# Performance work log

Measured on AMD Instinct MI355X. Metric: run time of the kernel, lower is better.

The kernel has to match this reference:

```python
import jax, jax.numpy as jnp
import numpy as np

N_ENT = 40000      # n_ent_vocab
NUM_POS = 24       # n_rel_vocab // 2
N_REL = 48         # n_rel_vocab (fwd + inverse relations)
BODY_LEN = 3
N_EDGES = 300000
BATCH = 64
THR = 1e-20


def setup_inputs() -> dict:
    key = jax.random.key(0)
    ks = jax.random.split(key, 8)
    return {
        "q_head": jax.random.randint(ks[0], (BATCH,), 0, N_ENT, dtype=jnp.int32),
        "q_rel": jax.random.randint(ks[1], (BATCH,), 0, NUM_POS, dtype=jnp.int32),
        "t": jax.random.randint(ks[2], (BATCH,), 0, N_ENT, dtype=jnp.int32),
        # dec_output is a softmax over relations -> positive weights in (0,1)
        "attention": jax.random.uniform(ks[3], (BATCH, BODY_LEN, N_REL), dtype=jnp.float32),
        "edge_head": jax.random.randint(ks[4], (N_EDGES,), 0, N_ENT, dtype=jnp.int32),
        "edge_tail": jax.random.randint(ks[5], (N_EDGES,), 0, N_ENT, dtype=jnp.int32),
        "edge_rel": jax.random.randint(ks[6], (N_EDGES,), 0, NUM_POS, dtype=jnp.int32),
        # uncertain-KG confidence values stored in the sparse adjacency
        "edge_val": jax.random.uniform(ks[7], (N_EDGES,), dtype=jnp.float32),
    }


def reference(q_head, q_rel, t, attention, edge_head, edge_tail, edge_rel, edge_val):
    """Fused equivalent of Translator.forwardAllNLP.

    database[r] are sparse [N_ENT, N_ENT] matrices; here the whole multigraph is
    one edge list (edge_head, edge_tail, edge_rel, edge_val). torch.sparse.mm
    per relation + attention-weighted accumulation becomes a single gather /
    segment_sum pass over all relations at once.
    """
    B = q_head.shape[0]
    # zero out the query triples in the (shared) database, as in the torch code
    killed = ((edge_head[None, :] == q_head[:, None])
              & (edge_tail[None, :] == t[:, None])
              & (edge_rel[None, :] == q_rel[:, None])).any(axis=0)
    vals = jnp.where(killed, 0.0, edge_val)  # [E]

    mem = jax.nn.one_hot(q_head, N_ENT, dtype=jnp.float32)  # [B, N_ENT]
    for step in range(BODY_LEN):
        attn = attention[:, step]                 # [B, N_REL]
        a_fwd = attn[:, edge_rel]                 # [B, E]  attention[:,step,r]
        a_rev = attn[:, edge_rel + NUM_POS]       # [B, E]  attention[:,step,r+num_pos]
        gh = mem[:, edge_head] * vals             # [B, E]  sparse.mm(mem, A_r)
        gt = mem[:, edge_tail] * vals             # [B, E]  sparse.mm(mem, A_r^T)
        fwd_msg = jax.ops.segment_sum((gh * a_fwd).T, edge_tail, num_segments=N_ENT).T
        rev_msg = jax.ops.segment_sum((gt * a_rev).T, edge_head, num_segments=N_ENT).T
        # self-loop term: memories * attention[:, step, -1]
        mem = fwd_msg + rev_msg + mem * attn[:, -1:]

    mem = mem / jnp.maximum(THR, mem.sum(axis=1, keepdims=True))
    # -sum(one_hot(t) * log(max(thr, mem))) == -log(max(thr, mem[b, t[b]]))
    tgt_prob = mem[jnp.arange(B), t]
    batch_loss = -jnp.log(jnp.maximum(THR, tgt_prob)).mean()
    return batch_loss, mem
```

## Files before the change

### kernel.cpp

```cpp
#include <hip/hip_runtime.h>
#include <hip/hip_bf16.h>

#define N_ENT 40000
#define NB 64
#define BODY_LEN 3
#define N_REL 48
#define NUM_POS 24
#define THR 1e-20f

#define SCAN_NBLK ((N_ENT + 255) / 256)


__global__ void k_zero(int* __restrict__ deg, int* __restrict__ fcnt,
                       float* __restrict__ sums) {
    int i = blockIdx.x * 256 + threadIdx.x;
    if (i < N_ENT) deg[i] = 0;
    if (i < 3) fcnt[i] = 0;
    if (i >= 64 && i < 128) sums[i - 64] = 0.0f;
}

__global__ void k_count(const int* __restrict__ eh, const int* __restrict__ et,
                        int* __restrict__ deg, int nE) {
    int i = blockIdx.x * 256 + threadIdx.x;
    if (i < nE) {
        atomicAdd(&deg[eh[i]], 1);
        atomicAdd(&deg[et[i]], 1);
    }
}

__global__ void k_blocksum(const int* __restrict__ deg, int* __restrict__ partial) {
    __shared__ int ws[4];
    int t = threadIdx.x;
    int i = blockIdx.x * 256 + t;
    int v = (i < N_ENT) ? deg[i] : 0;
#pragma unroll
    for (int off = 32; off > 0; off >>= 1) v += __shfl_down(v, off);
    if ((t & 63) == 0) ws[t >> 6] = v;
    __syncthreads();
    if (t == 0) partial[blockIdx.x] = ws[0] + ws[1] + ws[2] + ws[3];
}

__global__ void k_scan_small(const int* __restrict__ partial, int* __restrict__ pofs,
                             int* __restrict__ offs) {
    __shared__ int s[256];
    int t = threadIdx.x;
    int v = (t < SCAN_NBLK) ? partial[t] : 0;
    s[t] = v;
    __syncthreads();
    for (int off = 1; off < 256; off <<= 1) {
        int add = (t >= off) ? s[t - off] : 0;
        __syncthreads();
        s[t] += add;
        __syncthreads();
    }
    if (t < SCAN_NBLK) pofs[t] = s[t] - v;
    if (t == 255) offs[N_ENT] = s[255];
}

__global__ void k_offsets(const int* __restrict__ deg, const int* __restrict__ pofs,
                          int* __restrict__ offs, int* __restrict__ csrCur) {
    __shared__ int s[256];
    int t = threadIdx.x;
    int i = blockIdx.x * 256 + t;
    int v = (i < N_ENT) ? deg[i] : 0;
    s[t] = v;
    __syncthreads();
    for (int off = 1; off < 256; off <<= 1) {
        int add = (t >= off) ? s[t - off] : 0;
        __syncthreads();
        s[t] += add;
        __syncthreads();
    }
    if (i < N_ENT) {
        int ex = pofs[blockIdx.x] + s[t] - v;
        offs[i] = ex;
        csrCur[i] = ex;
    }
}

__global__ void k_scatter(const int* __restrict__ qh, const int* __restrict__ qr,
                          const int* __restrict__ tt, const int* __restrict__ eh,
                          const int* __restrict__ et, const int* __restrict__ er,
                          const float* __restrict__ ev, int* __restrict__ csrCur,
                          uint2* __restrict__ csr, int nE) {
    __shared__ long long s_key[NB];
    int tid = threadIdx.x;
    if (tid < NB)
        s_key[tid] = ((long long)qh[tid] << 32) | ((long long)tt[tid] << 8) | (long long)qr[tid];
    __syncthreads();
    int i = blockIdx.x * 256 + tid;
    if (i < nE) {
        int h = eh[i], t = et[i], r = er[i];
        long long k = ((long long)h << 32) | ((long long)t << 8) | (long long)r;
        bool killed = false;
#pragma unroll
        for (int b = 0; b < NB; ++b) killed |= (s_key[b] == k);
        float v = killed ? 0.0f : ev[i];
        unsigned vb = __float_as_uint(v);
        int sh = atomicAdd(&csrCur[h], 1);
        csr[sh] = make_uint2((unsigned)t | ((unsigned)r << 16), vb);
        int st = atomicAdd(&csrCur[t], 1);
        csr[st] = make_uint2((unsigned)h | ((unsigned)(r + NUM_POS) << 16), vb);
    }
}

#define DEC_BLOCKS 320
#define FLIST_LDS 192

__device__ __forceinline__ void flag_entities(unsigned long long m, int lane,
                                              int ent, int* s_cnt, int* s_list) {
    bool flag = ((lane & 15) == 0) && ((m >> lane) & 0xFFFFULL);
    unsigned long long am = __ballot(flag);
    if (am) {
        int leader = __ffsll((long long)am) - 1;
        int lb = 0;
        if (lane == leader) lb = atomicAdd(s_cnt, __popcll(am));
        lb = __shfl(lb, leader);
        if (flag) {
            int rank = __popcll(am & ((1ULL << lane) - 1ULL));
            s_list[lb + rank] = ent;
        }
    }
}

__global__ void k_init_decay(const int* __restrict__ qh, const float* __restrict__ attn,
                             float* __restrict__ nxt, int* __restrict__ fcnt,
                             int* __restrict__ flist) {
    __shared__ float s_d[NB];
    __shared__ int s_q[NB];
    __shared__ int s_list[FLIST_LDS];
    __shared__ int s_cnt, s_gbase;
    int tid = threadIdx.x;
    if (tid < NB) {
        s_d[tid] = attn[tid * (BODY_LEN * N_REL) + 0 * N_REL + (N_REL - 1)];
        s_q[tid] = qh[tid];
    }
    if (tid == 0) s_cnt = 0;
    __syncthreads();
    int lane = tid & 63;
    const int total4 = NB * N_ENT / 4;
    for (int i4 = blockIdx.x * 256 + tid; i4 < total4; i4 += gridDim.x * 256) {
        int ent = (i4 * 4) >> 6;
        int b0 = (i4 * 4) & 63;
        float4 w;
        w.x = (s_q[b0 + 0] == ent) ? s_d[b0 + 0] : 0.0f;
        w.y = (s_q[b0 + 1] == ent) ? s_d[b0 + 1] : 0.0f;
        w.z = (s_q[b0 + 2] == ent) ? s_d[b0 + 2] : 0.0f;
        w.w = (s_q[b0 + 3] == ent) ? s_d[b0 + 3] : 0.0f;
        ((float4*)nxt)[i4] = w;
        bool nz = (s_q[b0 + 0] == ent) | (s_q[b0 + 1] == ent) |
                  (s_q[b0 + 2] == ent) | (s_q[b0 + 3] == ent);
        unsigned long long m = __ballot(nz);
        flag_entities(m, lane, ent, &s_cnt, s_list);
    }
    __syncthreads();
    if (tid == 0 && s_cnt) s_gbase = atomicAdd(fcnt, s_cnt);
    __syncthreads();
    for (int i = tid; i < s_cnt; i += 256) flist[s_gbase + i] = s_list[i];
}

__global__ void k_decay(const float* __restrict__ oldm, float* __restrict__ nxt,
                        const float* __restrict__ attn, int step,
                        int* __restrict__ fcnt, int* __restrict__ flist) {
    __shared__ float s_d[NB];
    __shared__ int s_list[FLIST_LDS];
    __shared__ int s_cnt, s_gbase;
    int tid = threadIdx.x;
    if (tid < NB)
        s_d[tid] = attn[tid * (BODY_LEN * N_REL) + step * N_REL + (N_REL - 1)];
    if (tid == 0) s_cnt = 0;
    __syncthreads();
    int lane = tid & 63;
    const int total4 = NB * N_ENT / 4;
    for (int i4 = blockIdx.x * 256 + tid; i4 < total4; i4 += gridDim.x * 256) {
        float4 v = ((const float4*)oldm)[i4];
        int b0 = (tid * 4) & 63;
        float4 w;
        w.x = v.x * s_d[b0 + 0];
        w.y = v.y * s_d[b0 + 1];
        w.z = v.z * s_d[b0 + 2];
        w.w = v.w * s_d[b0 + 3];
        ((float4*)nxt)[i4] = w;
        bool nz = (v.x != 0.0f) | (v.y != 0.0f) | (v.z != 0.0f) | (v.w != 0.0f);
        unsigned long long m = __ballot(nz);
        flag_entities(m, lane, (i4 * 4) >> 6, &s_cnt, s_list);
    }
    __syncthreads();
    if (tid == 0 && s_cnt) s_gbase = atomicAdd(fcnt, s_cnt);
    __syncthreads();
    for (int i = tid; i < s_cnt; i += 256) flist[s_gbase + i] = s_list[i];
}

template <bool STEP0>
__global__ __launch_bounds__(256) void k_fstep(
    const uint2* __restrict__ csr, const int* __restrict__ offs,
    const int* __restrict__ flist, const int* __restrict__ fcnt,
    const float* __restrict__ attn, int step,
    const float* __restrict__ oldm, const int* __restrict__ qh,
    float* __restrict__ nxt) {
    __shared__ float s_attn[NB][N_REL + 1];
    int tid = threadIdx.x;
    for (int idx = tid; idx < NB * N_REL; idx += 256) {
        int b = idx / N_REL, r = idx % N_REL;
        s_attn[b][r] = attn[b * (BODY_LEN * N_REL) + step * N_REL + r];
    }
    __syncthreads();
    int lane = tid & 63;
    int myqh = STEP0 ? qh[lane] : 0;
    int n = *fcnt;
    int w = (blockIdx.x * 256 + tid) >> 6;
    int nW = (gridDim.x * 256) >> 6;
    for (int f = w; f < n; f += nW) {
        int e = flist[f];
        float src = STEP0 ? ((myqh == e) ? 1.0f : 0.0f)
                          : oldm[(size_t)e * 64 + lane];
        int base = offs[e];
        int cnt = offs[e + 1] - base;
        for (int k0 = 0; k0 < cnt; k0 += 64) {
            uint2 slot = make_uint2(0u, 0u);
            if (k0 + lane < cnt) slot = csr[base + k0 + lane];
            int lim = min(64, cnt - k0);
            for (int j = 0; j < lim; ++j) {
                unsigned meta = (unsigned)__shfl((int)slot.x, j);
                float v = __uint_as_float((unsigned)__shfl((int)slot.y, j));
                if (v == 0.0f) continue;
                float val = src * v * s_attn[lane][meta >> 16];
                if (val != 0.0f)
                    atomicAdd(&nxt[(size_t)(meta & 0xFFFFu) * 64 + lane], val);
            }
        }
    }
}

__global__ void k_sums(const float* __restrict__ mem, float* __restrict__ sums) {
    __shared__ float s_s[NB];
    if (threadIdx.x < NB) s_s[threadIdx.x] = 0.0f;
    __syncthreads();
    const float4* m4 = (const float4*)mem;
    const int total4 = NB * N_ENT / 4;
    float4 acc = {0.0f, 0.0f, 0.0f, 0.0f};
    for (int i = blockIdx.x * 256 + threadIdx.x; i < total4; i += gridDim.x * 256) {
        float4 v = m4[i];
        acc.x += v.x; acc.y += v.y; acc.z += v.z; acc.w += v.w;
    }
    int b0 = (threadIdx.x * 4) & 63;
    atomicAdd(&s_s[b0 + 0], acc.x);
    atomicAdd(&s_s[b0 + 1], acc.y);
    atomicAdd(&s_s[b0 + 2], acc.z);
    atomicAdd(&s_s[b0 + 3], acc.w);
    __syncthreads();
    if (threadIdx.x < NB) atomicAdd(&sums[threadIdx.x], s_s[threadIdx.x]);
}

__global__ void k_norm_tr(const float* __restrict__ mem, const float* __restrict__ sums,
                          const int* __restrict__ tt, float* __restrict__ out) {
    if (blockIdx.x == N_ENT / 64) {
        int b = threadIdx.x;
        if (b < 64) {
            float p = mem[(size_t)tt[b] * 64 + b] / fmaxf(THR, sums[b]);
            float l = -logf(fmaxf(THR, p));
#pragma unroll
            for (int off = 32; off > 0; off >>= 1) l += __shfl_down(l, off);
            if (b == 0) out[0] = l * (1.0f / 64.0f);
        }
        return;
    }
    __shared__ float tile[64][65];
    __shared__ float s_inv[64];
    int tid = threadIdx.x;
    int e0 = blockIdx.x * 64;
    if (tid < 64) s_inv[tid] = 1.0f / fmaxf(THR, sums[tid]);
    const float4* m4 = (const float4*)(mem + (size_t)e0 * 64);
#pragma unroll
    for (int k = 0; k < 4; ++k) {
        int i4 = k * 256 + tid;
        float4 v = m4[i4];
        int el = i4 >> 4, b0 = (i4 * 4) & 63;
        tile[el][b0 + 0] = v.x; tile[el][b0 + 1] = v.y;
        tile[el][b0 + 2] = v.z; tile[el][b0 + 3] = v.w;
    }
    __syncthreads();
#pragma unroll
    for (int k = 0; k < 16; ++k) {
        int idx = k * 256 + tid;
        int el = idx & 63, b = idx >> 6;
        out[1 + (size_t)b * N_ENT + e0 + el] = tile[el][b] * s_inv[b];
    }
}

extern "C" void kernel_launch(void* const* d_in, const int* in_sizes, int n_in,
                              void* d_out, int out_size, void* d_ws, size_t ws_size,
                              hipStream_t stream) {
    const int*   qh   = (const int*)d_in[0];
    const int*   qr   = (const int*)d_in[1];
    const int*   tt   = (const int*)d_in[2];
    const float* attn = (const float*)d_in[3];
    const int*   eh   = (const int*)d_in[4];
    const int*   et   = (const int*)d_in[5];
    const int*   er   = (const int*)d_in[6];
    const float* ev   = (const float*)d_in[7];
    float* out = (float*)d_out;
    int nE = in_sizes[4];

    const size_t MEM_BYTES = (size_t)NB * N_ENT * sizeof(float);
    char* ws = (char*)d_ws;
    int*   offs    = (int*)ws;
    int*   deg     = (int*)(ws + (192u << 10));
    int*   csrCur  = (int*)(ws + (384u << 10));
    int*   flist   = (int*)(ws + (576u << 10));
    int*   fcnt    = (int*)(ws + (768u << 10));
    float* sums    = (float*)(ws + (768u << 10) + 256);
    int*   partial = (int*)(ws + (768u << 10) + 4096);
    int*   pofs    = (int*)(ws + (768u << 10) + 8192);
    float* memA    = (float*)(ws + (1u << 20));
    float* memB;
    char*  csrBase;
    size_t csrBytes = (size_t)2 * nE * sizeof(uint2);
    size_t needBoth = (size_t)(1u << 20) + 2 * MEM_BYTES + csrBytes;
    if (ws_size >= needBoth) {
        memB = (float*)(ws + (1u << 20) + MEM_BYTES);
        csrBase = ws + (1u << 20) + 2 * MEM_BYTES;
    } else {
        memB = out + 1;
        csrBase = ws + (1u << 20) + MEM_BYTES;
    }
    uint2* csr = (uint2*)csrBase;

    const int EB = (nE + 255) / 256;

    k_zero<<<SCAN_NBLK, 256, 0, stream>>>(deg, fcnt, sums);
    k_count<<<EB, 256, 0, stream>>>(eh, et, deg, nE);
    k_blocksum<<<SCAN_NBLK, 256, 0, stream>>>(deg, partial);
    k_scan_small<<<1, 256, 0, stream>>>(partial, pofs, offs);
    k_offsets<<<SCAN_NBLK, 256, 0, stream>>>(deg, pofs, offs, csrCur);
    k_scatter<<<EB, 256, 0, stream>>>(qh, qr, tt, eh, et, er, ev, csrCur, csr, nE);

    k_init_decay<<<DEC_BLOCKS, 256, 0, stream>>>(qh, attn, memA, fcnt + 0, flist);
    k_fstep<true><<<16, 256, 0, stream>>>(csr, offs, flist, fcnt + 0, attn, 0,
                                          nullptr, qh, memA);
    float* curm = memA;
    float* nxtm = memB;
    for (int s = 1; s < BODY_LEN; ++s) {
        k_decay<<<DEC_BLOCKS, 256, 0, stream>>>(curm, nxtm, attn, s, fcnt + s, flist);
        k_fstep<false><<<1024, 256, 0, stream>>>(csr, offs, flist, fcnt + s, attn, s,
                                                 curm, nullptr, nxtm);
        float* tmp = curm; curm = nxtm; nxtm = tmp;
    }

    k_sums<<<128, 256, 0, stream>>>(curm, sums);
    k_norm_tr<<<N_ENT / 64 + 1, 256, 0, stream>>>(curm, sums, tt, out);
}
```

Measured before the change: 222.4 us.

## Build CSR via two-pass bucketed radix sort instead of global atomic scatter

Replaces the per-entity degree count, multi-kernel scan and global-atomic scatter with a two-pass bucket sort. Pass A bins edges into 157 buckets of 256 entities using block-local LDS histograms and one global atomic per bucket per block. Pass B sorts each bucket locally in LDS and writes the CSR offsets. This removes the contended global atomics and the random scattered writes, at the cost of an extra intermediate buffer and a second pass over the items.

Result: faster. 200.1 us (-10.0%).

```diff
diff --git a/kernel.cpp b/kernel.cpp
--- a/kernel.cpp
+++ b/kernel.cpp
@@ -1,5 +1,4 @@
 #include <hip/hip_runtime.h>
-#include <hip/hip_bf16.h>
 
 #define N_ENT 40000
 #define NB 64
@@ -8,43 +7,40 @@
 #define NUM_POS 24
 #define THR 1e-20f
 
-#define SCAN_NBLK ((N_ENT + 255) / 256)
-
-
-__global__ void k_zero(int* __restrict__ deg, int* __restrict__ fcnt,
+#define NBK 157
+#define PA_BLOCKS 320
+#define DEC_BLOCKS 320
+#define FLIST_LDS 192
+
+
+__global__ void k_zero(int* __restrict__ bktCnt, int* __restrict__ fcnt,
                        float* __restrict__ sums) {
-    int i = blockIdx.x * 256 + threadIdx.x;
-    if (i < N_ENT) deg[i] = 0;
-    if (i < 3) fcnt[i] = 0;
-    if (i >= 64 && i < 128) sums[i - 64] = 0.0f;
-}
-
-__global__ void k_count(const int* __restrict__ eh, const int* __restrict__ et,
-                        int* __restrict__ deg, int nE) {
-    int i = blockIdx.x * 256 + threadIdx.x;
-    if (i < nE) {
-        atomicAdd(&deg[eh[i]], 1);
-        atomicAdd(&deg[et[i]], 1);
-    }
-}
-
-__global__ void k_blocksum(const int* __restrict__ deg, int* __restrict__ partial) {
-    __shared__ int ws[4];
     int t = threadIdx.x;
-    int i = blockIdx.x * 256 + t;
-    int v = (i < N_ENT) ? deg[i] : 0;
-#pragma unroll
-    for (int off = 32; off > 0; off >>= 1) v += __shfl_down(v, off);
-    if ((t & 63) == 0) ws[t >> 6] = v;
-    __syncthreads();
-    if (t == 0) partial[blockIdx.x] = ws[0] + ws[1] + ws[2] + ws[3];
-}
-
-__global__ void k_scan_small(const int* __restrict__ partial, int* __restrict__ pofs,
-                             int* __restrict__ offs) {
+    if (t < NBK) bktCnt[t] = 0;
+    if (t < 3) fcnt[t] = 0;
+    if (t < NB) sums[t] = 0.0f;
+}
+
+__global__ void k_bhist(const int* __restrict__ eh, const int* __restrict__ et,
+                        int* __restrict__ bktCnt, int nE) {
+    __shared__ int h[NBK];
+    int tid = threadIdx.x;
+    for (int i = tid; i < NBK; i += 256) h[i] = 0;
+    __syncthreads();
+    for (int i = blockIdx.x * 256 + tid; i < nE; i += gridDim.x * 256) {
+        atomicAdd(&h[eh[i] >> 8], 1);
+        atomicAdd(&h[et[i] >> 8], 1);
+    }
+    __syncthreads();
+    for (int i = tid; i < NBK; i += 256)
+        if (h[i]) atomicAdd(&bktCnt[i], h[i]);
+}
+
+__global__ void k_bscan(const int* __restrict__ bktCnt, int* __restrict__ bktBase,
+                        int* __restrict__ bktCur, int* __restrict__ offs) {
     __shared__ int s[256];
     int t = threadIdx.x;
-    int v = (t < SCAN_NBLK) ? partial[t] : 0;
+    int v = (t < NBK) ? bktCnt[t] : 0;
     s[t] = v;
     __syncthreads();
     for (int off = 1; off < 256; off <<= 1) {
@@ -53,59 +49,97 @@
         s[t] += add;
         __syncthreads();
     }
-    if (t < SCAN_NBLK) pofs[t] = s[t] - v;
-    if (t == 255) offs[N_ENT] = s[255];
-}
-
-__global__ void k_offsets(const int* __restrict__ deg, const int* __restrict__ pofs,
-                          int* __restrict__ offs, int* __restrict__ csrCur) {
-    __shared__ int s[256];
-    int t = threadIdx.x;
-    int i = blockIdx.x * 256 + t;
-    int v = (i < N_ENT) ? deg[i] : 0;
-    s[t] = v;
-    __syncthreads();
-    for (int off = 1; off < 256; off <<= 1) {
-        int add = (t >= off) ? s[t - off] : 0;
-        __syncthreads();
-        s[t] += add;
-        __syncthreads();
-    }
-    if (i < N_ENT) {
-        int ex = pofs[blockIdx.x] + s[t] - v;
-        offs[i] = ex;
-        csrCur[i] = ex;
-    }
-}
-
-__global__ void k_scatter(const int* __restrict__ qh, const int* __restrict__ qr,
-                          const int* __restrict__ tt, const int* __restrict__ eh,
-                          const int* __restrict__ et, const int* __restrict__ er,
-                          const float* __restrict__ ev, int* __restrict__ csrCur,
-                          uint2* __restrict__ csr, int nE) {
+    if (t < NBK) {
+        int ex = s[t] - v;
+        bktBase[t] = ex;
+        bktCur[t] = ex;
+    }
+    if (t == NBK - 1) {
+        bktBase[NBK] = s[t];
+        offs[N_ENT] = s[t];
+    }
+}
+
+__global__ void k_passA(const int* __restrict__ qh, const int* __restrict__ qr,
+                        const int* __restrict__ tq, const int* __restrict__ eh,
+                        const int* __restrict__ et, const int* __restrict__ er,
+                        const float* __restrict__ ev, int* __restrict__ bktCur,
+                        uint2* __restrict__ items, int nE) {
     __shared__ long long s_key[NB];
+    __shared__ int h[NBK];
+    __shared__ int myB[NBK];
     int tid = threadIdx.x;
     if (tid < NB)
-        s_key[tid] = ((long long)qh[tid] << 32) | ((long long)tt[tid] << 8) | (long long)qr[tid];
-    __syncthreads();
-    int i = blockIdx.x * 256 + tid;
-    if (i < nE) {
-        int h = eh[i], t = et[i], r = er[i];
-        long long k = ((long long)h << 32) | ((long long)t << 8) | (long long)r;
+        s_key[tid] = ((long long)qh[tid] << 32) | ((long long)tq[tid] << 8) | (long long)qr[tid];
+    for (int i = tid; i < NBK; i += 256) h[i] = 0;
+    __syncthreads();
+    int chunk = (nE + PA_BLOCKS - 1) / PA_BLOCKS;
+    int b0 = blockIdx.x * chunk;
+    int b1 = min(nE, b0 + chunk);
+    for (int i = b0 + tid; i < b1; i += 256) {
+        atomicAdd(&h[eh[i] >> 8], 1);
+        atomicAdd(&h[et[i] >> 8], 1);
+    }
+    __syncthreads();
+    for (int i = tid; i < NBK; i += 256) {
+        int c = h[i];
+        myB[i] = c ? atomicAdd(&bktCur[i], c) : 0;
+        h[i] = 0;
+    }
+    __syncthreads();
+    for (int i = b0 + tid; i < b1; i += 256) {
+        int hh = eh[i], te = et[i], r = er[i];
+        long long k = ((long long)hh << 32) | ((long long)te << 8) | (long long)r;
         bool killed = false;
 #pragma unroll
         for (int b = 0; b < NB; ++b) killed |= (s_key[b] == k);
-        float v = killed ? 0.0f : ev[i];
-        unsigned vb = __float_as_uint(v);
-        int sh = atomicAdd(&csrCur[h], 1);
-        csr[sh] = make_uint2((unsigned)t | ((unsigned)r << 16), vb);
-        int st = atomicAdd(&csrCur[t], 1);
-        csr[st] = make_uint2((unsigned)h | ((unsigned)(r + NUM_POS) << 16), vb);
-    }
-}
-
-#define DEC_BLOCKS 320
-#define FLIST_LDS 192
+        unsigned vb = killed ? 0u : __float_as_uint(ev[i]);
+        int bk1 = hh >> 8;
+        int rk1 = atomicAdd(&h[bk1], 1);
+        items[myB[bk1] + rk1] =
+            make_uint2((unsigned)te | ((unsigned)r << 16) | ((unsigned)(hh & 255) << 24), vb);
+        int bk2 = te >> 8;
+        int rk2 = atomicAdd(&h[bk2], 1);
+        items[myB[bk2] + rk2] =
+            make_uint2((unsigned)hh | ((unsigned)(r + NUM_POS) << 16) | ((unsigned)(te & 255) << 24), vb);
+    }
+}
+
+__global__ void k_passB(const uint2* __restrict__ itemsA, const int* __restrict__ bktBase,
+                        int* __restrict__ offs, uint2* __restrict__ csr) {
+    __shared__ int cnt[256];
+    __shared__ int sc[256];
+    int tid = threadIdx.x;
+    int b = blockIdx.x;
+    int e0 = b << 8;
+    int eCnt = min(256, N_ENT - e0);
+    cnt[tid] = 0;
+    __syncthreads();
+    int ib = bktBase[b];
+    int n = bktBase[b + 1] - ib;
+    for (int i = tid; i < n; i += 256)
+        atomicAdd(&cnt[itemsA[ib + i].x >> 24], 1);
+    __syncthreads();
+    int v = cnt[tid];
+    sc[tid] = v;
+    __syncthreads();
+    for (int off = 1; off < 256; off <<= 1) {
+        int add = (tid >= off) ? sc[tid - off] : 0;
+        __syncthreads();
+        sc[tid] += add;
+        __syncthreads();
+    }
+    int ex = sc[tid] - v;
+    if (tid < eCnt) offs[e0 + tid] = ib + ex;
+    cnt[tid] = ex;
+    __syncthreads();
+    for (int i = tid; i < n; i += 256) {
+        uint2 it = itemsA[ib + i];
+        int k = (int)(it.x >> 24);
+        int p = atomicAdd(&cnt[k], 1);
+        csr[ib + p] = it;
+    }
+}
 
 __device__ __forceinline__ void flag_entities(unsigned long long m, int lane,
                                               int ent, int* s_cnt, int* s_list) {
@@ -224,7 +258,7 @@
                 unsigned meta = (unsigned)__shfl((int)slot.x, j);
                 float v = __uint_as_float((unsigned)__shfl((int)slot.y, j));
                 if (v == 0.0f) continue;
-                float val = src * v * s_attn[lane][meta >> 16];
+                float val = src * v * s_attn[lane][(meta >> 16) & 63];
                 if (val != 0.0f)
                     atomicAdd(&nxt[(size_t)(meta & 0xFFFFu) * 64 + lane], val);
             }
@@ -305,35 +339,31 @@
     const size_t MEM_BYTES = (size_t)NB * N_ENT * sizeof(float);
     char* ws = (char*)d_ws;
     int*   offs    = (int*)ws;
-    int*   deg     = (int*)(ws + (192u << 10));
-    int*   csrCur  = (int*)(ws + (384u << 10));
-    int*   flist   = (int*)(ws + (576u << 10));
-    int*   fcnt    = (int*)(ws + (768u << 10));
-    float* sums    = (float*)(ws + (768u << 10) + 256);
-    int*   partial = (int*)(ws + (768u << 10) + 4096);
-    int*   pofs    = (int*)(ws + (768u << 10) + 8192);
-    float* memA    = (float*)(ws + (1u << 20));
+    int*   flist   = (int*)(ws + (192u << 10));
+    int*   bktCnt  = (int*)(ws + (384u << 10));
+    int*   bktBase = (int*)(ws + (388u << 10));
+    int*   bktCur  = (int*)(ws + (392u << 10));
+    int*   fcnt    = (int*)(ws + (396u << 10));
+    float* sums    = (float*)(ws + (400u << 10));
+    uint2* csr     = (uint2*)(ws + (1u << 20));
+    float* memA    = (float*)(ws + (6u << 20));
     float* memB;
-    char*  csrBase;
-    size_t csrBytes = (size_t)2 * nE * sizeof(uint2);
-    size_t needBoth = (size_t)(1u << 20) + 2 * MEM_BYTES + csrBytes;
+    uint2* itemsA;
+    size_t itemsBytes = (size_t)2 * nE * sizeof(uint2);
+    size_t needBoth = (size_t)(6u << 20) + 2 * MEM_BYTES + itemsBytes;
     if (ws_size >= needBoth) {
-        memB = (float*)(ws + (1u << 20) + MEM_BYTES);
-        csrBase = ws + (1u << 20) + 2 * MEM_BYTES;
+        memB   = (float*)(ws + (6u << 20) + MEM_BYTES);
+        itemsA = (uint2*)(ws + (6u << 20) + 2 * MEM_BYTES);
     } else {
-        memB = out + 1;
-        csrBase = ws + (1u << 20) + MEM_BYTES;
-    }
-    uint2* csr = (uint2*)csrBase;
-
-    const int EB = (nE + 255) / 256;
-
-    k_zero<<<SCAN_NBLK, 256, 0, stream>>>(deg, fcnt, sums);
-    k_count<<<EB, 256, 0, stream>>>(eh, et, deg, nE);
-    k_blocksum<<<SCAN_NBLK, 256, 0, stream>>>(deg, partial);
-    k_scan_small<<<1, 256, 0, stream>>>(partial, pofs, offs);
-    k_offsets<<<SCAN_NBLK, 256, 0, stream>>>(deg, pofs, offs, csrCur);
-    k_scatter<<<EB, 256, 0, stream>>>(qh, qr, tt, eh, et, er, ev, csrCur, csr, nE);
+        memB   = out + 1;
+        itemsA = (uint2*)(out + 1);
+    }
+
+    k_zero<<<1, 256, 0, stream>>>(bktCnt, fcnt, sums);
+    k_bhist<<<PA_BLOCKS, 256, 0, stream>>>(eh, et, bktCnt, nE);
+    k_bscan<<<1, 256, 0, stream>>>(bktCnt, bktBase, bktCur, offs);
+    k_passA<<<PA_BLOCKS, 256, 0, stream>>>(qh, qr, tt, eh, et, er, ev, bktCur, itemsA, nE);
+    k_passB<<<NBK, 256, 0, stream>>>(itemsA, bktBase, offs, csr);
 
     k_init_decay<<<DEC_BLOCKS, 256, 0, stream>>>(qh, attn, memA, fcnt + 0, flist);
     k_fstep<true><<<16, 256, 0, stream>>>(csr, offs, flist, fcnt + 0, attn, 0,
```
